# Performance work log

Measured on AMD Instinct MI355X. Metric: run time of the kernel, lower is better.

## Reference

```python
import jax, jax.numpy as jnp
import numpy as np
from jax import lax

B, C, H, W = 8, 64, 64, 64
C8 = C // 8
EPS = 1e-5


def setup_inputs() -> dict:
    key = jax.random.key(0)
    ks = jax.random.split(key, 10)
    s = lambda *sh: 0.02
    inp = {
        "x": jax.random.normal(ks[0], (B, C, H, W), dtype=jnp.float32),
        "conv_b_w": jax.random.normal(ks[1], (C8, C), dtype=jnp.float32) * 0.05,
        "conv_b_b": jnp.zeros((C8,), jnp.float32),
        "conv_c_w": jax.random.normal(ks[2], (C8, C), dtype=jnp.float32) * 0.05,
        "conv_c_b": jnp.zeros((C8,), jnp.float32),
        "conv_d_w": jax.random.normal(ks[3], (C, C), dtype=jnp.float32) * 0.05,
        "conv_d_b": jnp.zeros((C,), jnp.float32),
        "alpha": jnp.zeros((1,), jnp.float32) + 0.1,  # learned PAM scale
        "beta": jnp.zeros((1,), jnp.float32) + 0.1,   # learned CAM scale
        "conv_w": jax.random.normal(ks[4], (2 * C, C, 3, 3), dtype=jnp.float32) * 0.02,
        "conv_bias": jnp.zeros((2 * C,), jnp.float32),
        "bn_gamma": jnp.ones((2 * C,), jnp.float32),
        "bn_beta": jnp.zeros((2 * C,), jnp.float32),
    }
    return inp


def _conv1x1(x, w, b):
    # x: [B,C,H,W], w: [O,C] -> [B,O,H,W]
    return jnp.einsum('oc,bchw->bohw', w, x) + b[None, :, None, None]


def _forward(x, conv_b_w, conv_b_b, conv_c_w, conv_c_b, conv_d_w, conv_d_b,
             alpha, beta, conv_w, conv_bias, bn_gamma, bn_beta):
    b, c, h, w = x.shape
    n = h * w
    # ---- Position Attention Module ----
    feat_b = _conv1x1(x, conv_b_w, conv_b_b).reshape(b, C8, n)   # [B,C8,N]
    feat_c = _conv1x1(x, conv_c_w, conv_c_b).reshape(b, C8, n)   # [B,C8,N]
    # torch: bmm(feat_b^T [B,N,C8], feat_c [B,C8,N]) -> [B,N,N]
    attn_s = jax.nn.softmax(jnp.einsum('bcn,bcm->bnm', feat_b, feat_c), axis=-1)
    feat_d = _conv1x1(x, conv_d_w, conv_d_b).reshape(b, c, n)    # [B,C,N]
    # torch: bmm(feat_d, attn_s^T) -> out[b,c,n] = sum_m feat_d[b,c,m]*attn[b,n,m]
    feat_e = jnp.einsum('bcm,bnm->bcn', feat_d, attn_s).reshape(b, c, h, w)
    x = alpha[0] * feat_e + x
    # ---- Channel Attention Module ----
    fa = x.reshape(b, c, n)                                      # [B,C,N]
    att = jnp.einsum('bcn,bdn->bcd', fa, fa)                     # [B,C,C]
    att_new = jnp.max(att, axis=-1, keepdims=True) - att
    att = jax.nn.softmax(att_new, axis=-1)
    fe = jnp.einsum('bcd,bdn->bcn', att, fa).reshape(b, c, h, w)
    x = beta[0] * fe + x
    # ---- conv3x3 + BN (batch stats) + ReLU + maxpool(2,2,pad=(1,0)) ----
    out = lax.conv_general_dilated(x, conv_w, (1, 1), ((1, 1), (1, 1)),
                                   dimension_numbers=('NCHW', 'OIHW', 'NCHW'))
    out = out + conv_bias[None, :, None, None]
    mean = jnp.mean(out, axis=(0, 2, 3), keepdims=True)
    var = jnp.var(out, axis=(0, 2, 3), keepdims=True)
    out = (out - mean) * lax.rsqrt(var + EPS)
    out = out * bn_gamma[None, :, None, None] + bn_beta[None, :, None, None]
    out = jax.nn.relu(out)
    # MaxPool2d(kernel=2, stride=2, padding=(1,0)): -inf padding on height only
    out = lax.reduce_window(out, -jnp.inf, lax.max,
                            (1, 1, 2, 2), (1, 1, 2, 2),
                            ((0, 0), (0, 0), (1, 1), (0, 0)))
    return out


def reference(x, conv_b_w, conv_b_b, conv_c_w, conv_c_b, conv_d_w, conv_d_b,
              alpha, beta, conv_w, conv_bias, bn_gamma, bn_beta):
    return _forward(x, conv_b_w, conv_b_b, conv_c_w, conv_c_b, conv_d_w, conv_d_b,
                    alpha, beta, conv_w, conv_bias, bn_gamma, bn_beta)
```

## Files before the change

### kernel.cpp

```cpp
#include <hip/hip_runtime.h>

using f32x4  = __attribute__((ext_vector_type(4))) float;
using bf16x8 = __attribute__((ext_vector_type(8))) short;
using u32x4  = __attribute__((ext_vector_type(4))) unsigned int;
using u32x2  = __attribute__((ext_vector_type(2))) unsigned int;
typedef unsigned short u16;

__device__ __forceinline__ u16 f2bf(float f) {
  unsigned u = __float_as_uint(f);
  unsigned r = (u + 0x7FFFu + ((u >> 16) & 1u)) >> 16;
  return (u16)r;
}

__global__ void __launch_bounds__(256) k1_conv1x1(
    const float* __restrict__ x, const float* __restrict__ wB, const float* __restrict__ bB,
    const float* __restrict__ wC, const float* __restrict__ bC,
    const float* __restrict__ wD, const float* __restrict__ bD,
    u16* __restrict__ featBb, u16* __restrict__ featCb, u16* __restrict__ featD,
    const float* __restrict__ cw, u16* __restrict__ wb) {
  const int t = threadIdx.x;
  const int b = blockIdx.y;
  const int z = blockIdx.z;
  if (z == 3) {
    int gid = (b * 16 + blockIdx.x) * 256 + t;
#pragma unroll
    for (int k = 0; k < 3; ++k) {
      int F = gid + k * 32768;
      if (F < 73728) {
        int j = F & 7, lane = (F >> 3) & 63, T = F >> 9;
        int tap = T >> 4, g = (T >> 1) & 7, kc = T & 1;
        int l16 = lane & 15, quad = lane >> 4;
        int oc = g * 16 + l16, ic = kc * 32 + quad * 8 + j;
        wb[F] = f2bf(cw[(oc * 64 + ic) * 9 + tap]);
      }
    }
    return;
  }
  __shared__ float W[2048];
  __shared__ float Bias[32];
  const int n = blockIdx.x * 256 + t;
  if (z == 0) {
    for (int i = t; i < 512; i += 256) W[i] = wB[i];
    for (int i = t; i < 512; i += 256) W[512 + i] = wC[i];
    if (t < 8) Bias[t] = bB[t];
    if (t >= 8 && t < 16) Bias[t] = bC[t - 8];
  } else {
    const float* wsrc = wD + (z - 1) * 2048;
    for (int i = t; i < 2048; i += 256) W[i] = wsrc[i];
    if (t < 32) Bias[t] = bD[(z - 1) * 32 + t];
  }
  __syncthreads();
  float xv[64];
#pragma unroll
  for (int c = 0; c < 64; ++c) xv[c] = x[((b * 64 + c) << 12) + n];
  if (z == 0) {
    float o[16];
#pragma unroll
    for (int k = 0; k < 16; ++k) {
      f32x4 s = {0.f, 0.f, 0.f, 0.f};
#pragma unroll
      for (int cq = 0; cq < 16; ++cq) {
        f32x4 wv = *(const f32x4*)&W[k * 64 + cq * 4];
        f32x4 xq = {xv[cq * 4], xv[cq * 4 + 1], xv[cq * 4 + 2], xv[cq * 4 + 3]};
        s += wv * xq;
      }
      o[k] = Bias[k] + s[0] + s[1] + s[2] + s[3];
    }
    int base = ((b << 12) + n) * 8;
    u32x4 pb, pc;
#pragma unroll
    for (int i = 0; i < 4; ++i) {
      pb[i] = (unsigned)f2bf(o[2 * i]) | ((unsigned)f2bf(o[2 * i + 1]) << 16);
      pc[i] = (unsigned)f2bf(o[8 + 2 * i]) | ((unsigned)f2bf(o[8 + 2 * i + 1]) << 16);
    }
    *(u32x4*)&featBb[base] = pb;
    *(u32x4*)&featCb[base] = pc;
  } else {
#pragma unroll 4
    for (int k = 0; k < 32; ++k) {
      f32x4 s = {0.f, 0.f, 0.f, 0.f};
#pragma unroll
      for (int cq = 0; cq < 16; ++cq) {
        f32x4 wv = *(const f32x4*)&W[k * 64 + cq * 4];
        f32x4 xq = {xv[cq * 4], xv[cq * 4 + 1], xv[cq * 4 + 2], xv[cq * 4 + 3]};
        s += wv * xq;
      }
      float val = Bias[k] + s[0] + s[1] + s[2] + s[3];
      featD[((b * 64 + (z - 1) * 32 + k) << 12) + n] = f2bf(val);
    }
  }
}

__global__ void __launch_bounds__(256) k2_pam_part(
    const u16* __restrict__ fBb, const u16* __restrict__ fCb, const u16* __restrict__ fD,
    u16* __restrict__ numPart, float* __restrict__ denPart) {
  __shared__ u16 Kf[128 * 8];
  __shared__ u16 Df[64 * 132];
  __shared__ u16 Ps4[4][4][16 * 72];
  const int t = threadIdx.x, b = blockIdx.y, z = blockIdx.z;
  const int w = t >> 6, lane = t & 63, quad = lane >> 4, l16 = lane & 15;
  const int nb = blockIdx.x * 256 + w * 64;
  u16* myPs = &Ps4[w][0][0];

  bf16x8 bq[4];
#pragma unroll
  for (int j = 0; j < 4; ++j) {
    bq[j] = *(const bf16x8*)&fBb[(((b << 12) + nb + j * 16 + l16) << 3)];
    if (quad != 0) bq[j] = (bf16x8)(short)0;
  }

  f32x4 acc[4][4];
#pragma unroll
  for (int ct = 0; ct < 4; ++ct)
#pragma unroll
    for (int j = 0; j < 4; ++j) acc[ct][j] = (f32x4){0.f, 0.f, 0.f, 0.f};
  float denp[4] = {0.f, 0.f, 0.f, 0.f};
  const int mz = z << 10;

  for (int ch = 0; ch < 8; ++ch) {
    const int m0 = mz + (ch << 7);
    __syncthreads();
    if (t < 128) *(u32x4*)&Kf[t * 8] = *(const u32x4*)&fCb[(((b << 12) + m0 + t) << 3)];
#pragma unroll
    for (int h = 0; h < 4; ++h) {
      int idx = h * 256 + t;
      int r = idx >> 4, mo = (idx & 15) << 3;
      *(u32x4*)&Df[r * 132 + mo] = *(const u32x4*)&fD[((b * 64 + r) << 12) + m0 + mo];
    }
    __syncthreads();
#pragma unroll
    for (int sub = 0; sub < 2; ++sub) {
      const int ms = sub * 64;
#pragma unroll
      for (int mt = 0; mt < 4; ++mt) {
        bf16x8 af = *(const bf16x8*)&Kf[(ms + mt * 16 + l16) * 8];
#pragma unroll
        for (int j = 0; j < 4; ++j) {
          f32x4 zero = {0.f, 0.f, 0.f, 0.f};
          f32x4 s = __builtin_amdgcn_mfma_f32_16x16x32_bf16(af, bq[j], zero, 0, 0, 0);
          float e0 = __expf(s[0]), e1 = __expf(s[1]), e2 = __expf(s[2]), e3 = __expf(s[3]);
          denp[j] += (e0 + e1) + (e2 + e3);
          u32x2 pk;
          pk[0] = __builtin_amdgcn_perm(__float_as_uint(e1), __float_as_uint(e0), 0x07060302u);
          pk[1] = __builtin_amdgcn_perm(__float_as_uint(e3), __float_as_uint(e2), 0x07060302u);
          *(u32x2*)&myPs[j * 1152 + l16 * 72 + mt * 16 + quad * 4] = pk;
        }
      }
#pragma unroll
      for (int kc = 0; kc < 2; ++kc) {
        bf16x8 bv[4];
#pragma unroll
        for (int j = 0; j < 4; ++j)
          bv[j] = *(const bf16x8*)&myPs[j * 1152 + l16 * 72 + kc * 32 + quad * 8];
#pragma unroll
        for (int ct = 0; ct < 4; ++ct) {
          bf16x8 av = *(const bf16x8*)&Df[(ct * 16 + l16) * 132 + ms + kc * 32 + quad * 8];
#pragma unroll
          for (int j = 0; j < 4; ++j)
            acc[ct][j] = __builtin_amdgcn_mfma_f32_16x16x32_bf16(av, bv[j], acc[ct][j], 0, 0, 0);
        }
      }
    }
  }
#pragma unroll
  for (int j = 0; j < 4; ++j) {
    denp[j] += __shfl_xor(denp[j], 16);
    denp[j] += __shfl_xor(denp[j], 32);
  }
  const int zb = z * 8 + b;
#pragma unroll
  for (int ct = 0; ct < 4; ++ct)
#pragma unroll
    for (int j = 0; j < 4; ++j)
#pragma unroll
      for (int r = 0; r < 4; ++r) {
        int c = ct * 16 + quad * 4 + r;
        numPart[((zb * 64 + c) << 12) + nb + j * 16 + l16] = (u16)(__float_as_uint(acc[ct][j][r]) >> 16);
      }
  if (quad == 0)
#pragma unroll
    for (int j = 0; j < 4; ++j) denPart[(zb << 12) + nb + j * 16 + l16] = denp[j];
}

__global__ void __launch_bounds__(256) k3_gram(
    const u16* __restrict__ numPart, const float* __restrict__ denPart,
    const float* __restrict__ x, const float* __restrict__ alpha,
    float* __restrict__ x1, float* __restrict__ attPart) {
  __shared__ float X[64 * 132];
  __shared__ float Dinv[128];
  const int t = threadIdx.x, b = blockIdx.y, cx = blockIdx.x;
  const int n0 = cx * 128;
  if (t < 128) {
    float den = 0.f;
#pragma unroll
    for (int z = 0; z < 4; ++z) den += denPart[(((z * 8 + b) << 12)) + n0 + t];
    Dinv[t] = alpha[0] / den;
  }
  __syncthreads();
  for (int idx = t; idx < 4096; idx += 256) {
    int row = idx >> 6, cp = (idx & 63) * 2;
    int gi = ((b * 64 + row) << 12) + n0 + cp;
    float num0 = 0.f, num1 = 0.f;
#pragma unroll
    for (int z = 0; z < 4; ++z) {
      unsigned v = *(const unsigned*)&numPart[(((z * 8 + b) * 64 + row) << 12) + n0 + cp];
      num0 += __uint_as_float(v << 16);
      num1 += __uint_as_float(v & 0xFFFF0000u);
    }
    float v0 = num0 * Dinv[cp] + x[gi];
    float v1 = num1 * Dinv[cp + 1] + x[gi + 1];
    X[row * 132 + cp] = v0;
    X[row * 132 + cp + 1] = v1;
    x1[gi] = v0;
    x1[gi + 1] = v1;
  }
  __syncthreads();
  const int cg = t >> 4, dg = t & 15;
  f32x4 acc[4][4];
#pragma unroll
  for (int i = 0; i < 4; ++i)
#pragma unroll
    for (int k = 0; k < 4; ++k) acc[i][k] = (f32x4){0.f, 0.f, 0.f, 0.f};
  for (int nq0 = 0; nq0 < 32; ++nq0) {
    int nq = (nq0 + dg) & 31;
    f32x4 a[4], bb[4];
#pragma unroll
    for (int i = 0; i < 4; ++i) a[i] = *(const f32x4*)&X[(cg * 4 + i) * 132 + nq * 4];
#pragma unroll
    for (int k = 0; k < 4; ++k) bb[k] = *(const f32x4*)&X[(dg * 4 + k) * 132 + nq * 4];
#pragma unroll
    for (int i = 0; i < 4; ++i)
#pragma unroll
      for (int k = 0; k < 4; ++k) acc[i][k] += a[i] * bb[k];
  }
#pragma unroll
  for (int i = 0; i < 4; ++i)
#pragma unroll
    for (int k = 0; k < 4; ++k) {
      f32x4 s = acc[i][k];
      attPart[((b * 32 + cx) * 64 + cg * 4 + i) * 64 + dg * 4 + k] = s[0] + s[1] + s[2] + s[3];
    }
}

__global__ void __launch_bounds__(256) k4_softmax(const float* __restrict__ attPart, float* __restrict__ attP) {
  const int b = blockIdx.y, t = threadIdx.x;
  const int c = (blockIdx.x << 2) + (t >> 6), d = t & 63;
  float v = 0.f;
  for (int p = 0; p < 32; ++p) v += attPart[((b * 32 + p) * 64 + c) * 64 + d];
  float mn = v;
#pragma unroll
  for (int off = 1; off < 64; off <<= 1) mn = fminf(mn, __shfl_xor(mn, off));
  float e = __expf(mn - v);
  float sum = e;
#pragma unroll
  for (int off = 1; off < 64; off <<= 1) sum += __shfl_xor(sum, off);
  attP[(b * 64 + c) * 64 + d] = e / sum;
}

__global__ void __launch_bounds__(256) k5_apply(
    const float* __restrict__ attP, const float* __restrict__ x1,
    const float* __restrict__ beta, u16* __restrict__ x2b) {
  __shared__ float A[64 * 68];
  const int t = threadIdx.x, b = blockIdx.y;
  for (int idx = t; idx < 4096; idx += 256) A[(idx >> 6) * 68 + (idx & 63)] = attP[(b << 12) + idx];
  __syncthreads();
  const int n = blockIdx.x * 256 + t;
  float xv[64];
#pragma unroll
  for (int d = 0; d < 64; ++d) xv[d] = x1[((b * 64 + d) << 12) + n];
  const float bv = beta[0];
  u16* orow = x2b + (((size_t)(b << 12) + n) << 6);
#pragma unroll 2
  for (int cg = 0; cg < 8; ++cg) {
    unsigned pk[4];
#pragma unroll
    for (int ci = 0; ci < 8; ++ci) {
      int c = cg * 8 + ci;
      f32x4 s = {0.f, 0.f, 0.f, 0.f};
#pragma unroll
      for (int dq = 0; dq < 16; ++dq) {
        f32x4 avv = *(const f32x4*)&A[c * 68 + dq * 4];
        f32x4 xq = {xv[dq * 4], xv[dq * 4 + 1], xv[dq * 4 + 2], xv[dq * 4 + 3]};
        s += avv * xq;
      }
      float fe = s[0] + s[1] + s[2] + s[3];
      float val = bv * fe + xv[c];
      unsigned h = f2bf(val);
      if ((ci & 1) == 0) pk[ci >> 1] = h;
      else pk[ci >> 1] |= h << 16;
    }
    *(u32x4*)&orow[cg * 8] = (u32x4){pk[0], pk[1], pk[2], pk[3]};
  }
}

__global__ void __launch_bounds__(256) k6_mfma(const u16* __restrict__ x2b, const u16* __restrict__ wb,
                                               float* __restrict__ y) {
  __shared__ u16 Xl[3 * 66 * 72];
  const int t = threadIdx.x, b = blockIdx.y, h = blockIdx.x;
  for (int idx = t; idx < 3 * 66 * 8; idx += 256) {
    int r = idx / 528;
    int rem = idx - r * 528;
    int c = rem >> 3, icq = rem & 7;
    int gy = h - 1 + r, gx = c - 1;
    u32x4 v = {0u, 0u, 0u, 0u};
    if (gy >= 0 && gy < 64 && gx >= 0 && gx < 64)
      v = *(const u32x4*)&x2b[(((size_t)(b << 6 | gy) << 6) + gx) * 64 + icq * 8];
    *(u32x4*)&Xl[(r * 66 + c) * 72 + icq * 8] = v;
  }
  __syncthreads();
  const int w = t >> 6, lane = t & 63, quad = lane >> 4, l16 = lane & 15;
  const int mBase = (w & 1) * 64;
  const int og = (w & 1) * 4;
  const int nBase = (w >> 1) * 32;
  f32x4 acc[4][2];
#pragma unroll
  for (int ot = 0; ot < 4; ++ot)
#pragma unroll
    for (int nt = 0; nt < 2; ++nt) acc[ot][nt] = (f32x4){0.f, 0.f, 0.f, 0.f};
#pragma unroll 3
  for (int tap = 0; tap < 9; ++tap) {
    const int dy = tap / 3, dx = tap - dy * 3;
    bf16x8 af[4][2];
#pragma unroll
    for (int ot = 0; ot < 4; ++ot)
#pragma unroll
      for (int kc = 0; kc < 2; ++kc)
        af[ot][kc] = *(const bf16x8*)&wb[((((tap * 8 + og + ot) * 2 + kc) << 6) + lane) << 3];
#pragma unroll
    for (int nt = 0; nt < 2; ++nt) {
      const int prow = dy * 66 + nBase + nt * 16 + l16 + dx;
#pragma unroll
      for (int kc = 0; kc < 2; ++kc) {
        bf16x8 bv = *(const bf16x8*)&Xl[prow * 72 + kc * 32 + quad * 8];
#pragma unroll
        for (int ot = 0; ot < 4; ++ot)
          acc[ot][nt] = __builtin_amdgcn_mfma_f32_16x16x32_bf16(af[ot][kc], bv, acc[ot][nt], 0, 0, 0);
      }
    }
  }
#pragma unroll
  for (int ot = 0; ot < 4; ++ot)
#pragma unroll
    for (int nt = 0; nt < 2; ++nt)
#pragma unroll
      for (int r = 0; r < 4; ++r) {
        int oc = mBase + ot * 16 + quad * 4 + r;
        int pix = nBase + nt * 16 + l16;
        y[((b * 128 + oc) << 12) + (h << 6) + pix] = acc[ot][nt][r];
      }
}

__global__ void __launch_bounds__(256) k7_part(const float* __restrict__ y, float* __restrict__ pstats) {
  const int ch = blockIdx.x, q = blockIdx.y, t = threadIdx.x;
  float s = 0.f, ss = 0.f;
#pragma unroll
  for (int bb = 0; bb < 2; ++bb) {
    const float* p = y + (((q * 2 + bb) * 128 + ch) << 12);
#pragma unroll
    for (int i = 0; i < 16; ++i) { float v = p[i * 256 + t]; s += v; ss += v * v; }
  }
#pragma unroll
  for (int off = 1; off < 64; off <<= 1) { s += __shfl_xor(s, off); ss += __shfl_xor(ss, off); }
  __shared__ float rs[4], rss[4];
  if ((t & 63) == 0) { rs[t >> 6] = s; rss[t >> 6] = ss; }
  __syncthreads();
  if (t == 0) {
    pstats[ch * 8 + q * 2]     = rs[0] + rs[1] + rs[2] + rs[3];
    pstats[ch * 8 + q * 2 + 1] = rss[0] + rss[1] + rss[2] + rss[3];
  }
}

__global__ void __launch_bounds__(256) k8_pool(const float* __restrict__ y, const float* __restrict__ pstats,
                                               const float* __restrict__ gamma, const float* __restrict__ bbeta,
                                               float* __restrict__ out) {
  const int bc = blockIdx.x;
  const int ch = bc & 127;
  float S = 0.f, SS = 0.f;
#pragma unroll
  for (int q = 0; q < 4; ++q) { S += pstats[ch * 8 + q * 2]; SS += pstats[ch * 8 + q * 2 + 1]; }
  const float mean = S * (1.f / 32768.f);
  const float var = SS * (1.f / 32768.f) - mean * mean;
  const float sc = gamma[ch] * rsqrtf(var + 1e-5f);
  const float sh = bbeta[ch] - mean * sc;
  const float* p = y + (bc << 12);
  float* op = out + bc * (33 * 32);
  for (int i = threadIdx.x; i < 33 * 32; i += 256) {
    int oh = i >> 5, ow = i & 31;
    int r0 = 2 * oh - 1, r1 = 2 * oh;
    float m = 0.f;
    if (r0 >= 0) {
      m = fmaxf(m, p[r0 * 64 + 2 * ow] * sc + sh);
      m = fmaxf(m, p[r0 * 64 + 2 * ow + 1] * sc + sh);
    }
    if (r1 <= 63) {
      m = fmaxf(m, p[r1 * 64 + 2 * ow] * sc + sh);
      m = fmaxf(m, p[r1 * 64 + 2 * ow + 1] * sc + sh);
    }
    op[i] = m;
  }
}

extern "C" void kernel_launch(void* const* d_in, const int* in_sizes, int n_in,
                              void* d_out, int out_size, void* d_ws, size_t ws_size,
                              hipStream_t stream) {
  const float* x      = (const float*)d_in[0];
  const float* wB     = (const float*)d_in[1];
  const float* bB     = (const float*)d_in[2];
  const float* wC     = (const float*)d_in[3];
  const float* bC     = (const float*)d_in[4];
  const float* wD     = (const float*)d_in[5];
  const float* bD     = (const float*)d_in[6];
  const float* alpha  = (const float*)d_in[7];
  const float* beta   = (const float*)d_in[8];
  const float* cw     = (const float*)d_in[9];
  const float* gamma  = (const float*)d_in[11];
  const float* bnbeta = (const float*)d_in[12];

  char* ws = (char*)d_ws;
  u16*   featBb  = (u16*)  (ws + 0);
  u16*   featCb  = (u16*)  (ws + 524288);
  u16*   fDb     = (u16*)  (ws + 1048576);
  u16*   x2b     = (u16*)  (ws + 0);
  float* x1      = (float*)(ws + 5242880);
  u16*   numPart = (u16*)  (ws + 13631488);
  float* y       = (float*)(ws + 13631488);
  float* denPart = (float*)(ws + 30408704);
  float* attPart = (float*)(ws + 30932992);
  float* attP    = (float*)(ws + 35127296);
  u16*   wb      = (u16*)  (ws + 35258368);
  float* pstats  = (float*)(ws + 35405824);
  float* outp    = (float*)d_out;

  k1_conv1x1<<<dim3(16, 8, 4), 256, 0, stream>>>(x, wB, bB, wC, bC, wD, bD, featBb, featCb, fDb, cw, wb);
  k2_pam_part<<<dim3(16, 8, 4), 256, 0, stream>>>(featBb, featCb, fDb, numPart, denPart);
  k3_gram<<<dim3(32, 8), 256, 0, stream>>>(numPart, denPart, x, alpha, x1, attPart);
  k4_softmax<<<dim3(16, 8), 256, 0, stream>>>(attPart, attP);
  k5_apply<<<dim3(16, 8), 256, 0, stream>>>(attP, x1, beta, x2b);
  k6_mfma<<<dim3(64, 8), 256, 0, stream>>>(x2b, wb, y);
  k7_part<<<dim3(128, 4), 256, 0, stream>>>(y, pstats);
  k8_pool<<<dim3(1024), 256, 0, stream>>>(y, pstats, gamma, bnbeta, outp);
}
```

Baseline: 219.4 us.

## Pre-swizzle PAM key and value tensors into MFMA fragment layout, drop LDS staging

Result: slower. 244.8 us (+11.6%).

```diff
diff --git a/kernel.cpp b/kernel.cpp
--- a/kernel.cpp
+++ b/kernel.cpp
@@ -16,7 +16,7 @@
     const float* __restrict__ x, const float* __restrict__ wB, const float* __restrict__ bB,
     const float* __restrict__ wC, const float* __restrict__ bC,
     const float* __restrict__ wD, const float* __restrict__ bD,
-    u16* __restrict__ featBb, u16* __restrict__ featCb, u16* __restrict__ featD,
+    u16* __restrict__ featBb, u16* __restrict__ fCt, u16* __restrict__ fDt,
     const float* __restrict__ cw, u16* __restrict__ wb) {
   const int t = threadIdx.x;
   const int b = blockIdx.y;
@@ -74,7 +74,12 @@
       pc[i] = (unsigned)f2bf(o[8 + 2 * i]) | ((unsigned)f2bf(o[8 + 2 * i + 1]) << 16);
     }
     *(u32x4*)&featBb[base] = pb;
-    *(u32x4*)&featCb[base] = pc;
+    u16* ct0 = fCt + (size_t)(((((b << 8) | (n >> 4)) << 6) | (n & 15)) * 8);
+    u32x4 zz = {0u, 0u, 0u, 0u};
+    *(u32x4*)&ct0[0] = pc;
+    *(u32x4*)&ct0[16 * 8] = zz;
+    *(u32x4*)&ct0[32 * 8] = zz;
+    *(u32x4*)&ct0[48 * 8] = zz;
   } else {
 #pragma unroll 4
     for (int k = 0; k < 32; ++k) {
@@ -86,16 +91,17 @@
         s += wv * xq;
       }
       float val = Bias[k] + s[0] + s[1] + s[2] + s[3];
-      featD[((b * 64 + (z - 1) * 32 + k) << 12) + n] = f2bf(val);
+      int c = (z - 1) * 32 + k;
+      int elem = (((((b << 7) | (n >> 5)) << 2) | (c >> 4)) << 6 |
+                  ((c & 15) + (((n >> 3) & 3) << 4))) * 8 + (n & 7);
+      fDt[elem] = f2bf(val);
     }
   }
 }
 
 __global__ void __launch_bounds__(256) k2_pam_part(
-    const u16* __restrict__ fBb, const u16* __restrict__ fCb, const u16* __restrict__ fD,
+    const u16* __restrict__ fBb, const u16* __restrict__ fCt, const u16* __restrict__ fDt,
     u16* __restrict__ numPart, float* __restrict__ denPart) {
-  __shared__ u16 Kf[128 * 8];
-  __shared__ u16 Df[64 * 132];
   __shared__ u16 Ps4[4][4][16 * 72];
   const int t = threadIdx.x, b = blockIdx.y, z = blockIdx.z;
   const int w = t >> 6, lane = t & 63, quad = lane >> 4, l16 = lane & 15;
@@ -104,10 +110,8 @@
 
   bf16x8 bq[4];
 #pragma unroll
-  for (int j = 0; j < 4; ++j) {
+  for (int j = 0; j < 4; ++j)
     bq[j] = *(const bf16x8*)&fBb[(((b << 12) + nb + j * 16 + l16) << 3)];
-    if (quad != 0) bq[j] = (bf16x8)(short)0;
-  }
 
   f32x4 acc[4][4];
 #pragma unroll
@@ -115,50 +119,38 @@
 #pragma unroll
     for (int j = 0; j < 4; ++j) acc[ct][j] = (f32x4){0.f, 0.f, 0.f, 0.f};
   float denp[4] = {0.f, 0.f, 0.f, 0.f};
-  const int mz = z << 10;
-
-  for (int ch = 0; ch < 8; ++ch) {
-    const int m0 = mz + (ch << 7);
-    __syncthreads();
-    if (t < 128) *(u32x4*)&Kf[t * 8] = *(const u32x4*)&fCb[(((b << 12) + m0 + t) << 3)];
-#pragma unroll
-    for (int h = 0; h < 4; ++h) {
-      int idx = h * 256 + t;
-      int r = idx >> 4, mo = (idx & 15) << 3;
-      *(u32x4*)&Df[r * 132 + mo] = *(const u32x4*)&fD[((b * 64 + r) << 12) + m0 + mo];
-    }
-    __syncthreads();
-#pragma unroll
-    for (int sub = 0; sub < 2; ++sub) {
-      const int ms = sub * 64;
-#pragma unroll
-      for (int mt = 0; mt < 4; ++mt) {
-        bf16x8 af = *(const bf16x8*)&Kf[(ms + mt * 16 + l16) * 8];
-#pragma unroll
-        for (int j = 0; j < 4; ++j) {
-          f32x4 zero = {0.f, 0.f, 0.f, 0.f};
-          f32x4 s = __builtin_amdgcn_mfma_f32_16x16x32_bf16(af, bq[j], zero, 0, 0, 0);
-          float e0 = __expf(s[0]), e1 = __expf(s[1]), e2 = __expf(s[2]), e3 = __expf(s[3]);
-          denp[j] += (e0 + e1) + (e2 + e3);
-          u32x2 pk;
-          pk[0] = __builtin_amdgcn_perm(__float_as_uint(e1), __float_as_uint(e0), 0x07060302u);
-          pk[1] = __builtin_amdgcn_perm(__float_as_uint(e3), __float_as_uint(e2), 0x07060302u);
-          *(u32x2*)&myPs[j * 1152 + l16 * 72 + mt * 16 + quad * 4] = pk;
-        }
-      }
-#pragma unroll
-      for (int kc = 0; kc < 2; ++kc) {
-        bf16x8 bv[4];
+
+  for (int sub = 0; sub < 16; ++sub) {
+    const int msub = (z << 4) + sub;
+#pragma unroll
+    for (int mt = 0; mt < 4; ++mt) {
+      const int m16 = (msub << 2) + mt;
+      bf16x8 af = *(const bf16x8*)&fCt[(size_t)(((((b << 8) | m16) << 6) | lane) * 8)];
+#pragma unroll
+      for (int j = 0; j < 4; ++j) {
+        f32x4 zero = {0.f, 0.f, 0.f, 0.f};
+        f32x4 s = __builtin_amdgcn_mfma_f32_16x16x32_bf16(af, bq[j], zero, 0, 0, 0);
+        float e0 = __expf(s[0]), e1 = __expf(s[1]), e2 = __expf(s[2]), e3 = __expf(s[3]);
+        denp[j] += (e0 + e1) + (e2 + e3);
+        u32x2 pk;
+        pk[0] = __builtin_amdgcn_perm(__float_as_uint(e1), __float_as_uint(e0), 0x07060302u);
+        pk[1] = __builtin_amdgcn_perm(__float_as_uint(e3), __float_as_uint(e2), 0x07060302u);
+        *(u32x2*)&myPs[j * 1152 + l16 * 72 + mt * 16 + quad * 4] = pk;
+      }
+    }
+#pragma unroll
+    for (int kc = 0; kc < 2; ++kc) {
+      const int m32 = (msub << 1) + kc;
+      bf16x8 bv[4];
+#pragma unroll
+      for (int j = 0; j < 4; ++j)
+        bv[j] = *(const bf16x8*)&myPs[j * 1152 + l16 * 72 + kc * 32 + quad * 8];
+#pragma unroll
+      for (int ct = 0; ct < 4; ++ct) {
+        bf16x8 av = *(const bf16x8*)&fDt[(size_t)(((((((b << 7) | m32) << 2) | ct) << 6) | lane) * 8)];
 #pragma unroll
         for (int j = 0; j < 4; ++j)
-          bv[j] = *(const bf16x8*)&myPs[j * 1152 + l16 * 72 + kc * 32 + quad * 8];
-#pragma unroll
-        for (int ct = 0; ct < 4; ++ct) {
-          bf16x8 av = *(const bf16x8*)&Df[(ct * 16 + l16) * 132 + ms + kc * 32 + quad * 8];
-#pragma unroll
-          for (int j = 0; j < 4; ++j)
-            acc[ct][j] = __builtin_amdgcn_mfma_f32_16x16x32_bf16(av, bv[j], acc[ct][j], 0, 0, 0);
-        }
+          acc[ct][j] = __builtin_amdgcn_mfma_f32_16x16x32_bf16(av, bv[j], acc[ct][j], 0, 0, 0);
       }
     }
   }
@@ -418,21 +410,21 @@
 
   char* ws = (char*)d_ws;
   u16*   featBb  = (u16*)  (ws + 0);
-  u16*   featCb  = (u16*)  (ws + 524288);
-  u16*   fDb     = (u16*)  (ws + 1048576);
+  u16*   fCt     = (u16*)  (ws + 524288);
+  u16*   fDt     = (u16*)  (ws + 2621440);
   u16*   x2b     = (u16*)  (ws + 0);
-  float* x1      = (float*)(ws + 5242880);
-  u16*   numPart = (u16*)  (ws + 13631488);
-  float* y       = (float*)(ws + 13631488);
-  float* denPart = (float*)(ws + 30408704);
-  float* attPart = (float*)(ws + 30932992);
-  float* attP    = (float*)(ws + 35127296);
-  u16*   wb      = (u16*)  (ws + 35258368);
-  float* pstats  = (float*)(ws + 35405824);
+  float* x1      = (float*)(ws + 6815744);
+  u16*   numPart = (u16*)  (ws + 15204352);
+  float* y       = (float*)(ws + 15204352);
+  float* denPart = (float*)(ws + 31981568);
+  float* attPart = (float*)(ws + 32505856);
+  float* attP    = (float*)(ws + 36700160);
+  u16*   wb      = (u16*)  (ws + 36831232);
+  float* pstats  = (float*)(ws + 36978688);
   float* outp    = (float*)d_out;
 
-  k1_conv1x1<<<dim3(16, 8, 4), 256, 0, stream>>>(x, wB, bB, wC, bC, wD, bD, featBb, featCb, fDb, cw, wb);
-  k2_pam_part<<<dim3(16, 8, 4), 256, 0, stream>>>(featBb, featCb, fDb, numPart, denPart);
+  k1_conv1x1<<<dim3(16, 8, 4), 256, 0, stream>>>(x, wB, bB, wC, bC, wD, bD, featBb, fCt, fDt, cw, wb);
+  k2_pam_part<<<dim3(16, 8, 4), 256, 0, stream>>>(featBb, fCt, fDt, numPart, denPart);
   k3_gram<<<dim3(32, 8), 256, 0, stream>>>(numPart, denPart, x, alpha, x1, attPart);
   k4_softmax<<<dim3(16, 8), 256, 0, stream>>>(attPart, attP);
   k5_apply<<<dim3(16, 8), 256, 0, stream>>>(attP, x1, beta, x2b);
```
